# Kernel optimization log

Hardware: AMD Instinct MI355X
Metric: run time of the kernel (lower is better)

The kernel has to match this reference:

```python
import jax, jax.numpy as jnp
import numpy as np

NUM_HEADS = 8
NUM_LEVELS = 4
NUM_POINTS = 4


def _grid_sample(v, grid):
    """Bilinear grid_sample, padding_mode='zeros', align_corners=False.
    v: (N, C, H, W), grid: (N, Hg, Wg, 2) with grid[...,0]=x, grid[...,1]=y in [-1,1].
    Returns (N, C, Hg, Wg)."""
    N, C, H, W = v.shape
    Hg, Wg = grid.shape[1], grid.shape[2]
    x = ((grid[..., 0] + 1.0) * W - 1.0) * 0.5
    y = ((grid[..., 1] + 1.0) * H - 1.0) * 0.5
    x0 = jnp.floor(x)
    y0 = jnp.floor(y)
    x1 = x0 + 1.0
    y1 = y0 + 1.0
    wx1 = x - x0
    wx0 = 1.0 - wx1
    wy1 = y - y0
    wy0 = 1.0 - wy1
    vf = v.reshape(N, C, H * W)

    def corner(xi, yi, w):
        valid = (xi >= 0) & (xi < W) & (yi >= 0) & (yi < H)
        xi_c = jnp.clip(xi, 0, W - 1).astype(jnp.int32)
        yi_c = jnp.clip(yi, 0, H - 1).astype(jnp.int32)
        idx = (yi_c * W + xi_c).reshape(N, 1, Hg * Wg)
        g = jnp.take_along_axis(vf, idx, axis=2).reshape(N, C, Hg, Wg)
        return g * (w * valid.astype(v.dtype))[:, None]

    return (corner(x0, y0, wx0 * wy0) + corner(x1, y0, wx1 * wy0)
            + corner(x0, y1, wx0 * wy1) + corner(x1, y1, wx1 * wy1))


def setup_inputs() -> dict:
    rng = jax.random.key(0)
    ks = jax.random.split(rng, 6)
    bs, num_q, embed = 1, 40000, 256
    num_kv = NUM_LEVELS * NUM_POINTS  # 16, enforced by the module's asserts
    return {
        "query": jax.random.normal(ks[0], (bs, num_q, embed), jnp.float32),
        "key": jax.random.normal(ks[1], (bs, num_kv, embed), jnp.float32),
        "value": jax.random.normal(ks[2], (bs, num_kv, embed), jnp.float32),
        "reference_points": jax.random.uniform(ks[3], (bs, num_q, NUM_LEVELS, 2), jnp.float32),
        "spatial_shapes": np.array([[1, 2], [2, 2], [2, 3], [1, 2]], dtype=np.int32),  # (h,w), sums to 16
        "W_so": jax.random.normal(ks[4], (embed, NUM_HEADS * NUM_LEVELS * NUM_POINTS * 2), jnp.float32) * 0.02,
        "b_so": jax.random.normal(ks[5], (NUM_HEADS * NUM_LEVELS * NUM_POINTS * 2,), jnp.float32) * 0.02,
    }


def reference(query, key, value, reference_points, spatial_shapes, W_so, b_so):
    b, nq, embed = query.shape
    h, l, p = NUM_HEADS, NUM_LEVELS, NUM_POINTS
    d = embed // h
    ss = np.asarray(spatial_shapes)  # static (l, 2) (h, w)

    # sampling offsets: (b, nq, h, p, l, 2)  -- note (p, l) order per the original view
    off = (query @ W_so + b_so).reshape(b, nq, h, p, l, 2)

    # NOTE: to_Q/to_K/to_V outputs are overwritten in the original (dead code);
    # attention uses the raw query/key reshaped per-head.
    q = query.reshape(b, nq, h, d)
    k = key.reshape(b, -1, h, d)
    v = value.reshape(b, -1, h, d)
    attn = jax.nn.softmax(jnp.einsum('bqhd,bkhd->bqhk', q, k), axis=-1)
    attn = attn.reshape(b, nq, h, l, p)

    # normalize offsets by (w, h) per level, add reference points, then
    # reinterpret (p, l) axes as (l, p) via a plain reshape (faithful to .view)
    norm = jnp.asarray(np.stack([ss[:, 1], ss[:, 0]], axis=-1), dtype=query.dtype)  # (l, 2)
    loc = reference_points[:, :, None, None, :, :] + off / norm  # (b, nq, h, p, l, 2)
    loc = loc.reshape(b, nq, h, l, p, 2)
    grids = 2.0 * loc - 1.0

    sampled = []
    start = 0
    for lev in range(l):
        H_, W_ = int(ss[lev, 0]), int(ss[lev, 1])
        v_l = v[:, start:start + H_ * W_].transpose(0, 2, 3, 1).reshape(b * h, d, H_, W_)
        start += H_ * W_
        g_l = grids[:, :, :, lev].transpose(0, 2, 1, 3, 4).reshape(b * h, nq, p, 2)
        sampled.append(_grid_sample(v_l, g_l))  # (b*h, d, nq, p)
    sampled = jnp.stack(sampled, axis=-2).reshape(b * h, d, nq, l * p)

    aw = attn.transpose(0, 2, 1, 3, 4).reshape(b * h, 1, nq, l * p)
    out = (sampled * aw).sum(-1).reshape(b, h * d, nq)
    return out.transpose(0, 2, 1)
```

## Files before the change

### kernel.cpp

```cpp
#include <hip/hip_runtime.h>
#include <hip/hip_bf16.h>
#include <stdint.h>


typedef __attribute__((ext_vector_type(8))) short short8;
typedef __attribute__((ext_vector_type(4))) float float4_;

#define LDSTR 40
#define SB_OFF 2560
#define SMEM_BYTES 23040

static __device__ __forceinline__ uint16_t f2bf(float f) {
    union { float f; uint32_t u; } a; a.f = f;
    uint32_t r = a.u + 0x7fffu + ((a.u >> 16) & 1u);
    return (uint16_t)(r >> 16);
}
static __device__ __forceinline__ float bf2f(uint16_t b) {
    union { uint32_t u; float f; } a; a.u = ((uint32_t)b) << 16;
    return a.f;
}

template <int H_, int W_, int ST_>
static __device__ __forceinline__ void scatter(float* ws, float a, float x, float y) {
    float x0f = floorf(x), y0f = floorf(y);
    float fx = x - x0f, fy = y - y0f;
    int ix0 = (int)x0f, iy0 = (int)y0f;
    float xc[W_], yc[H_];
#pragma unroll
    for (int cx = 0; cx < W_; ++cx)
        xc[cx] = (ix0 == cx) ? (1.f - fx) : ((ix0 + 1 == cx) ? fx : 0.f);
#pragma unroll
    for (int cy = 0; cy < H_; ++cy)
        yc[cy] = ((iy0 == cy) ? (1.f - fy) : ((iy0 + 1 == cy) ? fy : 0.f)) * a;
#pragma unroll
    for (int cy = 0; cy < H_; ++cy)
#pragma unroll
        for (int cx = 0; cx < W_; ++cx)
            ws[ST_ + cy * W_ + cx] += xc[cx] * yc[cy];
}

__global__ __launch_bounds__(256) void k_transpose(const float* __restrict__ W,
                                                   uint16_t* __restrict__ WTb) {
    int n = blockIdx.x, k = threadIdx.x;
    WTb[n * 256 + k] = f2bf(W[k * 256 + n]);
}

__global__ __launch_bounds__(256) void k_fused(const float* __restrict__ q,
                                               const float* __restrict__ key,
                                               const float* __restrict__ value,
                                               const float* __restrict__ refp,
                                               const uint16_t* __restrict__ WTb,
                                               const float* __restrict__ bso,
                                               float* __restrict__ out) {
    __shared__ __align__(16) char smem[SMEM_BYTES];
    short* sA = (short*)smem;
    short* sB = (short*)(smem + SB_OFF);

    int t = threadIdx.x;
    int w = t >> 6, l = t & 63;
    int g = l >> 4, lrow = l & 15, lk = g * 8;
    int qbase = blockIdx.x * 32;
    int h2 = t >> 5, ql = t & 31;
    int qa = qbase + ql;

    int ar = t >> 3, ak = t & 7;
    float4_ acc[2][4];
#pragma unroll
    for (int i = 0; i < 2; ++i)
#pragma unroll
        for (int j = 0; j < 4; ++j) acc[i][j] = (float4_)0.f;

    float4_ pa = *(const float4_*)(q + (size_t)(qbase + ar) * 256 + ak * 4);
    short8 pb[4];
#pragma unroll
    for (int j = 0; j < 4; ++j)
        pb[j] = *(const short8*)(WTb + t * 256 + j * 8);

    for (int ks = 0; ks < 8; ++ks) {
        __syncthreads();
        {
            uint32_t p0 = (uint32_t)f2bf(pa.x) | ((uint32_t)f2bf(pa.y) << 16);
            uint32_t p1 = (uint32_t)f2bf(pa.z) | ((uint32_t)f2bf(pa.w) << 16);
            uint32_t* dst = (uint32_t*)&sA[ar * LDSTR + ak * 4];
            dst[0] = p0; dst[1] = p1;
#pragma unroll
            for (int j = 0; j < 4; ++j)
                *(short8*)&sB[t * LDSTR + j * 8] = pb[j];
        }
        if (ks < 7) {
            pa = *(const float4_*)(q + (size_t)(qbase + ar) * 256 + (ks + 1) * 32 + ak * 4);
#pragma unroll
            for (int j = 0; j < 4; ++j)
                pb[j] = *(const short8*)(WTb + t * 256 + (ks + 1) * 32 + j * 8);
        }
        __syncthreads();
        short8 af[2], bf[4];
#pragma unroll
        for (int mi = 0; mi < 2; ++mi)
            af[mi] = *(const short8*)&sA[(mi * 16 + lrow) * LDSTR + lk];
#pragma unroll
        for (int ni = 0; ni < 4; ++ni)
            bf[ni] = *(const short8*)&sB[(w * 64 + ni * 16 + lrow) * LDSTR + lk];
#pragma unroll
        for (int mi = 0; mi < 2; ++mi)
#pragma unroll
            for (int ni = 0; ni < 4; ++ni)
                acc[mi][ni] = __builtin_amdgcn_mfma_f32_16x16x32_bf16(
                    af[mi], bf[ni], acc[mi][ni], 0, 0, 0);
    }
    __syncthreads();

#pragma unroll
    for (int mi = 0; mi < 2; ++mi)
#pragma unroll
        for (int ni = 0; ni < 4; ++ni) {
            int col = w * 64 + ni * 16 + lrow;
            float b = bso[col];
            int qrow = mi * 16 + g * 4;
#pragma unroll
            for (int r = 0; r < 4; ++r) {
                int row = qrow + r;
                *(uint16_t*)(smem + row * 512 + ((col * 2) ^ ((row & 7) << 4))) =
                    f2bf(acc[mi][ni][r] + b);
            }
        }

    float sc[16];
#pragma unroll
    for (int kk = 0; kk < 16; ++kk) sc[kk] = 0.f;
#pragma unroll
    for (int half = 0; half < 2; ++half) {
        const float4_* qp = (const float4_*)(q + (size_t)qa * 256 + h2 * 32 + half * 16);
        float4_ qv[4];
#pragma unroll
        for (int j = 0; j < 4; ++j) qv[j] = qp[j];
#pragma unroll
        for (int kk = 0; kk < 16; ++kk) {
            const float4_* kp = (const float4_*)(key + kk * 256 + h2 * 32 + half * 16);
            float a = 0.f;
#pragma unroll
            for (int j = 0; j < 4; ++j) {
                float4_ kv = kp[j];
                a += qv[j].x * kv.x + qv[j].y * kv.y + qv[j].z * kv.z + qv[j].w * kv.w;
            }
            sc[kk] += a;
        }
    }
    {
        float m = sc[0];
#pragma unroll
        for (int kk = 1; kk < 16; ++kk) m = fmaxf(m, sc[kk]);
        float s = 0.f;
#pragma unroll
        for (int kk = 0; kk < 16; ++kk) { sc[kk] = __expf(sc[kk] - m); s += sc[kk]; }
        float inv = 1.f / s;
#pragma unroll
        for (int kk = 0; kk < 16; ++kk) sc[kk] *= inv;
    }
    __syncthreads();

    float4_ r01 = *(const float4_*)(refp + (size_t)qa * 8);
    float4_ r23 = *(const float4_*)(refp + (size_t)qa * 8 + 4);
    float rx[4] = {r01.x, r01.z, r23.x, r23.z};
    float ry[4] = {r01.y, r01.w, r23.y, r23.w};

    float ws[14];
#pragma unroll
    for (int j = 0; j < 14; ++j) ws[j] = 0.f;

#define SAMPLE_PT(J, PP, GH, GW, ST, NW, NH)                                  \
    {                                                                         \
        float ox = bf2f((uint16_t)ovl.s[2 * (J)]);                            \
        float oy = bf2f((uint16_t)ovl.s[2 * (J) + 1]);                        \
        float x = (rx[PP] + ox * (NW)) * (float)(GW)-0.5f;                    \
        float y = (ry[PP] + oy * (NH)) * (float)(GH)-0.5f;                    \
        scatter<GH, GW, ST>(ws, sc[4 * LEV + (J)], x, y);                     \
    }
    {
        union OvU { short8 v; short s[8]; } ovl;
#define LEV 0
        ovl.v = *(const short8*)(smem + ql * 512 + ((h2 * 64 + LEV * 16) ^ ((ql & 7) << 4)));
        SAMPLE_PT(0, 0, 1, 2, 0, 0.5f, 1.0f)
        SAMPLE_PT(1, 1, 1, 2, 0, 0.5f, 0.5f)
        SAMPLE_PT(2, 2, 1, 2, 0, (1.f / 3.f), 0.5f)
        SAMPLE_PT(3, 3, 1, 2, 0, 0.5f, 1.0f)
#undef LEV
#define LEV 1
        ovl.v = *(const short8*)(smem + ql * 512 + ((h2 * 64 + LEV * 16) ^ ((ql & 7) << 4)));
        SAMPLE_PT(0, 0, 2, 2, 2, 0.5f, 1.0f)
        SAMPLE_PT(1, 1, 2, 2, 2, 0.5f, 0.5f)
        SAMPLE_PT(2, 2, 2, 2, 2, (1.f / 3.f), 0.5f)
        SAMPLE_PT(3, 3, 2, 2, 2, 0.5f, 1.0f)
#undef LEV
#define LEV 2
        ovl.v = *(const short8*)(smem + ql * 512 + ((h2 * 64 + LEV * 16) ^ ((ql & 7) << 4)));
        SAMPLE_PT(0, 0, 2, 3, 6, 0.5f, 1.0f)
        SAMPLE_PT(1, 1, 2, 3, 6, 0.5f, 0.5f)
        SAMPLE_PT(2, 2, 2, 3, 6, (1.f / 3.f), 0.5f)
        SAMPLE_PT(3, 3, 2, 3, 6, 0.5f, 1.0f)
#undef LEV
#define LEV 3
        ovl.v = *(const short8*)(smem + ql * 512 + ((h2 * 64 + LEV * 16) ^ ((ql & 7) << 4)));
        SAMPLE_PT(0, 0, 1, 2, 12, 0.5f, 1.0f)
        SAMPLE_PT(1, 1, 1, 2, 12, 0.5f, 0.5f)
        SAMPLE_PT(2, 2, 1, 2, 12, (1.f / 3.f), 0.5f)
        SAMPLE_PT(3, 3, 1, 2, 12, 0.5f, 1.0f)
#undef LEV
    }
#undef SAMPLE_PT

    __syncthreads();

    {
        union PkU { uint32_t u[8]; short8 v2[2]; } pk;
#pragma unroll
        for (int j = 0; j < 7; ++j)
            pk.u[j] = (uint32_t)f2bf(ws[2 * j]) | ((uint32_t)f2bf(ws[2 * j + 1]) << 16);
        pk.u[7] = 0;
        *(short8*)(smem + t * 48)      = pk.v2[0];
        *(short8*)(smem + t * 48 + 16) = pk.v2[1];
    }
    __syncthreads();

    {
        union ZU { uint32_t u[4]; short8 v; } az;
        az.u[0] = 0; az.u[1] = 0; az.u[2] = 0; az.u[3] = 0;
#pragma unroll
        for (int hh = 0; hh < 2; ++hh) {
            int h = 2 * w + hh;
            union VbU { short8 v; uint16_t u[8]; } vb[2];
#pragma unroll
            for (int nt = 0; nt < 2; ++nt) {
                if (g < 2) {
                    int col = h * 32 + nt * 16 + lrow;
#pragma unroll
                    for (int j = 0; j < 8; ++j)
                        vb[nt].u[j] = f2bf(value[(g * 8 + j) * 256 + col]);
                } else {
                    vb[nt].v = az.v;
                }
            }
            float4_ acc2[2][2];
#pragma unroll
            for (int i = 0; i < 2; ++i)
#pragma unroll
                for (int j = 0; j < 2; ++j) acc2[i][j] = (float4_)0.f;
#pragma unroll
            for (int mt = 0; mt < 2; ++mt) {
                short8 af = (g < 2)
                    ? *(const short8*)(smem + (h * 32 + mt * 16 + lrow) * 48 + g * 16)
                    : az.v;
#pragma unroll
                for (int nt = 0; nt < 2; ++nt)
                    acc2[mt][nt] = __builtin_amdgcn_mfma_f32_16x16x32_bf16(
                        af, vb[nt].v, acc2[mt][nt], 0, 0, 0);
            }
#pragma unroll
            for (int mt = 0; mt < 2; ++mt)
#pragma unroll
                for (int nt = 0; nt < 2; ++nt)
#pragma unroll
                    for (int r = 0; r < 4; ++r)
                        out[(size_t)(qbase + mt * 16 + g * 4 + r) * 256
                            + h * 32 + nt * 16 + lrow] = acc2[mt][nt][r];
        }
    }
}

extern "C" void kernel_launch(void* const* d_in, const int* in_sizes, int n_in,
                              void* d_out, int out_size, void* d_ws, size_t ws_size,
                              hipStream_t stream) {
    (void)in_sizes; (void)n_in; (void)out_size; (void)ws_size;
    const float* query = (const float*)d_in[0];
    const float* key   = (const float*)d_in[1];
    const float* value = (const float*)d_in[2];
    const float* refp  = (const float*)d_in[3];
    const float* Wso   = (const float*)d_in[5];
    const float* bso   = (const float*)d_in[6];
    uint16_t* WTb = (uint16_t*)d_ws;

    hipLaunchKernelGGL(k_transpose, dim3(256), dim3(256), 0, stream, Wso, WTb);
    hipLaunchKernelGGL(k_fused, dim3(1250), dim3(256), 0, stream,
                       query, key, value, refp, WTb, bso, (float*)d_out);
}
```

Measured before the change: 72.73 us.

## Split fused kernel into projection/softmax kernel and sampling kernel via global scratch

Splits the single fused kernel into k1, which computes the bf16 sampling-offset GEMM and the softmax attention weights and writes both to workspace, and k2, which reads them back to do the bilinear scatter and the value contraction. The weight matrix is pre-laid-out in MFMA fragment order so k1 loads its B operands straight from global memory, and A fragments are read directly from the query, removing the LDS staging and barriers from the GEMM loop. The aim is to cut shared-memory use and synchronisation and raise occupancy. In exchange it adds an extra launch and roughly 30 MB of global round-trip traffic for the intermediates.

```diff
diff --git a/kernel.cpp b/kernel.cpp
--- a/kernel.cpp
+++ b/kernel.cpp
@@ -6,9 +6,8 @@
 typedef __attribute__((ext_vector_type(8))) short short8;
 typedef __attribute__((ext_vector_type(4))) float float4_;
 
-#define LDSTR 40
-#define SB_OFF 2560
-#define SMEM_BYTES 23040
+#define OFF_G_OFF 131072
+#define WG_G_OFF  (131072 + 40000 * 512)
 
 static __device__ __forceinline__ uint16_t f2bf(float f) {
     union { float f; uint32_t u; } a; a.f = f;
@@ -39,68 +38,55 @@
             ws[ST_ + cy * W_ + cx] += xc[cx] * yc[cy];
 }
 
-__global__ __launch_bounds__(256) void k_transpose(const float* __restrict__ W,
-                                                   uint16_t* __restrict__ WTb) {
-    int n = blockIdx.x, k = threadIdx.x;
-    WTb[n * 256 + k] = f2bf(W[k * 256 + n]);
-}
-
-__global__ __launch_bounds__(256) void k_fused(const float* __restrict__ q,
-                                               const float* __restrict__ key,
-                                               const float* __restrict__ value,
-                                               const float* __restrict__ refp,
-                                               const uint16_t* __restrict__ WTb,
-                                               const float* __restrict__ bso,
-                                               float* __restrict__ out) {
-    __shared__ __align__(16) char smem[SMEM_BYTES];
-    short* sA = (short*)smem;
-    short* sB = (short*)(smem + SB_OFF);
-
+__global__ __launch_bounds__(256) void k_prep(const float* __restrict__ W,
+                                              uint16_t* __restrict__ tab) {
+    int f = blockIdx.x * 256 + threadIdx.x;
+    int l = f & 63, nt = (f >> 6) & 15, ks = (f >> 10) & 7;
+    int col = nt * 16 + (l & 15);
+    int kb = ks * 32 + (l >> 4) * 8;
+    uint16_t* dst = tab + (size_t)f * 8;
+#pragma unroll
+    for (int j = 0; j < 8; ++j) dst[j] = f2bf(W[(size_t)(kb + j) * 256 + col]);
+}
+
+__global__ __launch_bounds__(256) void k1(const float* __restrict__ q,
+                                          const float* __restrict__ key,
+                                          const uint16_t* __restrict__ Wfrag,
+                                          const float* __restrict__ bso,
+                                          uint16_t* __restrict__ off_g,
+                                          float* __restrict__ wg_g) {
     int t = threadIdx.x;
     int w = t >> 6, l = t & 63;
-    int g = l >> 4, lrow = l & 15, lk = g * 8;
+    int g = l >> 4, lrow = l & 15;
     int qbase = blockIdx.x * 32;
     int h2 = t >> 5, ql = t & 31;
     int qa = qbase + ql;
 
-    int ar = t >> 3, ak = t & 7;
     float4_ acc[2][4];
 #pragma unroll
     for (int i = 0; i < 2; ++i)
 #pragma unroll
         for (int j = 0; j < 4; ++j) acc[i][j] = (float4_)0.f;
 
-    float4_ pa = *(const float4_*)(q + (size_t)(qbase + ar) * 256 + ak * 4);
-    short8 pb[4];
-#pragma unroll
-    for (int j = 0; j < 4; ++j)
-        pb[j] = *(const short8*)(WTb + t * 256 + j * 8);
-
+#pragma unroll
     for (int ks = 0; ks < 8; ++ks) {
-        __syncthreads();
-        {
-            uint32_t p0 = (uint32_t)f2bf(pa.x) | ((uint32_t)f2bf(pa.y) << 16);
-            uint32_t p1 = (uint32_t)f2bf(pa.z) | ((uint32_t)f2bf(pa.w) << 16);
-            uint32_t* dst = (uint32_t*)&sA[ar * LDSTR + ak * 4];
-            dst[0] = p0; dst[1] = p1;
-#pragma unroll
-            for (int j = 0; j < 4; ++j)
-                *(short8*)&sB[t * LDSTR + j * 8] = pb[j];
-        }
-        if (ks < 7) {
-            pa = *(const float4_*)(q + (size_t)(qbase + ar) * 256 + (ks + 1) * 32 + ak * 4);
-#pragma unroll
-            for (int j = 0; j < 4; ++j)
-                pb[j] = *(const short8*)(WTb + t * 256 + (ks + 1) * 32 + j * 8);
-        }
-        __syncthreads();
         short8 af[2], bf[4];
 #pragma unroll
-        for (int mi = 0; mi < 2; ++mi)
-            af[mi] = *(const short8*)&sA[(mi * 16 + lrow) * LDSTR + lk];
+        for (int mi = 0; mi < 2; ++mi) {
+            const float4_* ap = (const float4_*)(q
+                + (size_t)(qbase + mi * 16 + lrow) * 256 + ks * 32 + g * 8);
+            float4_ a0 = ap[0], a1 = ap[1];
+            union { uint32_t u[4]; short8 v; } pk;
+            pk.u[0] = (uint32_t)f2bf(a0.x) | ((uint32_t)f2bf(a0.y) << 16);
+            pk.u[1] = (uint32_t)f2bf(a0.z) | ((uint32_t)f2bf(a0.w) << 16);
+            pk.u[2] = (uint32_t)f2bf(a1.x) | ((uint32_t)f2bf(a1.y) << 16);
+            pk.u[3] = (uint32_t)f2bf(a1.z) | ((uint32_t)f2bf(a1.w) << 16);
+            af[mi] = pk.v;
+        }
 #pragma unroll
         for (int ni = 0; ni < 4; ++ni)
-            bf[ni] = *(const short8*)&sB[(w * 64 + ni * 16 + lrow) * LDSTR + lk];
+            bf[ni] = *(const short8*)(Wfrag
+                + ((size_t)(ks * 16 + w * 4 + ni) * 64 + l) * 8);
 #pragma unroll
         for (int mi = 0; mi < 2; ++mi)
 #pragma unroll
@@ -108,7 +94,6 @@
                 acc[mi][ni] = __builtin_amdgcn_mfma_f32_16x16x32_bf16(
                     af[mi], bf[ni], acc[mi][ni], 0, 0, 0);
     }
-    __syncthreads();
 
 #pragma unroll
     for (int mi = 0; mi < 2; ++mi)
@@ -116,13 +101,10 @@
         for (int ni = 0; ni < 4; ++ni) {
             int col = w * 64 + ni * 16 + lrow;
             float b = bso[col];
-            int qrow = mi * 16 + g * 4;
-#pragma unroll
-            for (int r = 0; r < 4; ++r) {
-                int row = qrow + r;
-                *(uint16_t*)(smem + row * 512 + ((col * 2) ^ ((row & 7) << 4))) =
+#pragma unroll
+            for (int r = 0; r < 4; ++r)
+                off_g[(size_t)(qbase + mi * 16 + g * 4 + r) * 256 + col] =
                     f2bf(acc[mi][ni][r] + b);
-            }
         }
 
     float sc[16];
@@ -157,7 +139,33 @@
 #pragma unroll
         for (int kk = 0; kk < 16; ++kk) sc[kk] *= inv;
     }
-    __syncthreads();
+#pragma unroll
+    for (int kk = 0; kk < 16; ++kk)
+        wg_g[(size_t)qa * 128 + h2 * 16 + kk] = sc[kk];
+}
+
+__global__ __launch_bounds__(256) void k2(const float* __restrict__ refp,
+                                          const uint16_t* __restrict__ off_g,
+                                          const float* __restrict__ wg_g,
+                                          const float* __restrict__ value,
+                                          float* __restrict__ out) {
+    __shared__ __align__(16) char smem[12288];
+    int t = threadIdx.x;
+    int w = t >> 6, l = t & 63;
+    int g = l >> 4, lrow = l & 15;
+    int qbase = blockIdx.x * 32;
+    int h2 = t >> 5, ql = t & 31;
+    int qa = qbase + ql;
+
+    float sc[16];
+    {
+        const float4_* sp = (const float4_*)(wg_g + (size_t)qa * 128 + h2 * 16);
+#pragma unroll
+        for (int j = 0; j < 4; ++j) {
+            float4_ v = sp[j];
+            sc[4 * j] = v.x; sc[4 * j + 1] = v.y; sc[4 * j + 2] = v.z; sc[4 * j + 3] = v.w;
+        }
+    }
 
     float4_ r01 = *(const float4_*)(refp + (size_t)qa * 8);
     float4_ r23 = *(const float4_*)(refp + (size_t)qa * 8 + 4);
@@ -178,29 +186,30 @@
     }
     {
         union OvU { short8 v; short s[8]; } ovl;
+        const short8* ob = (const short8*)(off_g + (size_t)qa * 256 + h2 * 32);
 #define LEV 0
-        ovl.v = *(const short8*)(smem + ql * 512 + ((h2 * 64 + LEV * 16) ^ ((ql & 7) << 4)));
+        ovl.v = ob[LEV];
         SAMPLE_PT(0, 0, 1, 2, 0, 0.5f, 1.0f)
         SAMPLE_PT(1, 1, 1, 2, 0, 0.5f, 0.5f)
         SAMPLE_PT(2, 2, 1, 2, 0, (1.f / 3.f), 0.5f)
         SAMPLE_PT(3, 3, 1, 2, 0, 0.5f, 1.0f)
 #undef LEV
 #define LEV 1
-        ovl.v = *(const short8*)(smem + ql * 512 + ((h2 * 64 + LEV * 16) ^ ((ql & 7) << 4)));
+        ovl.v = ob[LEV];
         SAMPLE_PT(0, 0, 2, 2, 2, 0.5f, 1.0f)
         SAMPLE_PT(1, 1, 2, 2, 2, 0.5f, 0.5f)
         SAMPLE_PT(2, 2, 2, 2, 2, (1.f / 3.f), 0.5f)
         SAMPLE_PT(3, 3, 2, 2, 2, 0.5f, 1.0f)
 #undef LEV
 #define LEV 2
-        ovl.v = *(const short8*)(smem + ql * 512 + ((h2 * 64 + LEV * 16) ^ ((ql & 7) << 4)));
+        ovl.v = ob[LEV];
         SAMPLE_PT(0, 0, 2, 3, 6, 0.5f, 1.0f)
         SAMPLE_PT(1, 1, 2, 3, 6, 0.5f, 0.5f)
         SAMPLE_PT(2, 2, 2, 3, 6, (1.f / 3.f), 0.5f)
         SAMPLE_PT(3, 3, 2, 3, 6, 0.5f, 1.0f)
 #undef LEV
 #define LEV 3
-        ovl.v = *(const short8*)(smem + ql * 512 + ((h2 * 64 + LEV * 16) ^ ((ql & 7) << 4)));
+        ovl.v = ob[LEV];
         SAMPLE_PT(0, 0, 1, 2, 12, 0.5f, 1.0f)
         SAMPLE_PT(1, 1, 1, 2, 12, 0.5f, 0.5f)
         SAMPLE_PT(2, 2, 1, 2, 12, (1.f / 3.f), 0.5f)
@@ -208,8 +217,6 @@
 #undef LEV
     }
 #undef SAMPLE_PT
-
-    __syncthreads();
 
     {
         union PkU { uint32_t u[8]; short8 v2[2]; } pk;
@@ -277,9 +284,14 @@
     const float* refp  = (const float*)d_in[3];
     const float* Wso   = (const float*)d_in[5];
     const float* bso   = (const float*)d_in[6];
-    uint16_t* WTb = (uint16_t*)d_ws;
-
-    hipLaunchKernelGGL(k_transpose, dim3(256), dim3(256), 0, stream, Wso, WTb);
-    hipLaunchKernelGGL(k_fused, dim3(1250), dim3(256), 0, stream,
-                       query, key, value, refp, WTb, bso, (float*)d_out);
-}
+    char* ws = (char*)d_ws;
+    uint16_t* Wfrag = (uint16_t*)ws;
+    uint16_t* off_g = (uint16_t*)(ws + OFF_G_OFF);
+    float*    wg_g  = (float*)(ws + WG_G_OFF);
+
+    hipLaunchKernelGGL(k_prep, dim3(32), dim3(256), 0, stream, Wso, Wfrag);
+    hipLaunchKernelGGL(k1, dim3(1250), dim3(256), 0, stream,
+                       query, key, Wfrag, bso, off_g, wg_g);
+    hipLaunchKernelGGL(k2, dim3(1250), dim3(256), 0, stream,
+                       refp, off_g, wg_g, value, (float*)d_out);
+}
```

Measured after the change: 80.74 us. 11.0% more time.
